# Optimization experiments

Hardware: AMD Instinct MI355X
Metric: run time of the kernel (lower is better)

Reference implementation:

```python
import jax, jax.numpy as jnp
import numpy as np

B, T, D, E = 2, 1653, 512, 8
D_E = D // E
BE = B * E


def setup_inputs() -> dict:
    key = jax.random.key(0)
    ks = jax.random.split(key, 11)
    s = 0.02  # keep linear-layer scale sane
    return {
        "input": jax.random.normal(ks[0], (B, T, D), jnp.float32),
        "Wq": jax.random.normal(ks[1], (D, D), jnp.float32) * s,
        "bq": jax.random.normal(ks[2], (D,), jnp.float32) * s,
        "Wk": jax.random.normal(ks[3], (D, D), jnp.float32) * s,
        "bk": jax.random.normal(ks[4], (D,), jnp.float32) * s,
        "Wv": jax.random.normal(ks[5], (D, D), jnp.float32) * s,
        "bv": jax.random.normal(ks[6], (D,), jnp.float32) * s,
        "Wo": jax.random.normal(ks[7], (D, D), jnp.float32) * s,
        "bo": jax.random.normal(ks[8], (D,), jnp.float32) * s,
        # random 'gaussian orthogonal punishment' matrix (diag(norms) @ blockwise-QR in torch; random here)
        "punish": jax.random.normal(ks[9], (T, T), jnp.float32) * (1.0 / np.sqrt(T)),
        # random tensor produced by torch.nn.init.orthogonal_(att_score) in the source
        "att_orth": jax.random.normal(ks[10], (BE, T, T), jnp.float32) * (1.0 / np.sqrt(T)),
    }


def _learnable_sigmoid(x):
    return 1.2 / (1.0 + jnp.exp(-1.6 * x))


def reference(input, Wq, bq, Wk, bk, Wv, bv, Wo, bo, punish, att_orth):
    # torch nn.Linear: y = x @ W^T + b
    def proj(W, b):
        # [B,T,D] -> permute(0,2,1) -> [B,D,T] -> reshape to [B*E, T, D_E]
        y = jnp.einsum('btd,ed->bte', input, W) + b
        return y.transpose(0, 2, 1).reshape(BE, T, D_E)

    Q = _learnable_sigmoid(proj(Wq, bq))            # [BE, T, D_E] (mask_q is all-ones => no-op)
    K = _learnable_sigmoid(proj(Wk, bk))            # [BE, T, D_E]
    V = proj(Wv, bv)                                # [BE, T, D_E]

    inv_sqrt_T = 1.0 / jnp.sqrt(jnp.float32(T))
    att = jnp.einsum('btd,bsd->bts', Q, K) * inv_sqrt_T  # [BE, T, T]

    # punishment: elementwise mul by broadcast punish matrix, then matmul with
    # the (transposed) random orthogonal tensor: att = (att * P) @ orth^T
    att = (att * punish[None, :, :]) @ att_orth.transpose(0, 2, 1)  # [BE, T, T]

    att = jnp.where(att == 0.0, jnp.float32(-2e20), att)  # masked_fill(att==0, -2e20)

    out = jnp.einsum('bts,bsd->btd', att, V)        # [BE, T, D_E]
    # permute(0,2,1) -> [BE, D_E, T] -> reshape [B, D, T] -> permute -> [B, T, D]
    out = out.transpose(0, 2, 1).reshape(B, D, T).transpose(0, 2, 1)
    return jnp.einsum('btd,ed->bte', out, Wo) + bo   # [B, T, D]
```

## Files before the change

kernel.cpp:

```cpp
#include <hip/hip_runtime.h>

#define TT 1653
#define DD 512
#define BB 2
#define DE 64
#define BEH 16
#define TTILES 26
#define TPAD 1664
#define SQN 26
#define NJC 4
#define MPSTRIDE TPAD

typedef __attribute__((ext_vector_type(8))) short bf16x8;
typedef __attribute__((ext_vector_type(4))) float f32x4;
typedef float f32x4u  __attribute__((ext_vector_type(4), aligned(4)));

__device__ __forceinline__ short f2bf(float f) {
    union { float f; unsigned u; } v; v.f = f;
    unsigned r = v.u + 0x7fffu + ((v.u >> 16) & 1u);
    return (short)(r >> 16);
}
__device__ __forceinline__ unsigned pack2(float a, float b) {
    return (unsigned)(unsigned short)f2bf(a) | ((unsigned)(unsigned short)f2bf(b) << 16);
}
__device__ __forceinline__ float bf2f(short s) {
    union { unsigned u; float f; } v; v.u = ((unsigned)(unsigned short)s) << 16;
    return v.f;
}

__global__ __launch_bounds__(256) void convp2_kernel(
    const float* __restrict__ P, short* __restrict__ Pbf)
{
    const int g = blockIdx.x * 256 + threadIdx.x;
    const int NG4 = TPAD / 4;
    if (g >= TT * NG4) return;
    const int r = g / NG4, c4 = (g - r * NG4) * 4;
    float p0 = 0.f, p1 = 0.f, p2 = 0.f, p3 = 0.f;
    const float* prow = P + (size_t)r * TT;
    if (c4 + 0 < TT) p0 = prow[c4 + 0];
    if (c4 + 1 < TT) p1 = prow[c4 + 1];
    if (c4 + 2 < TT) p2 = prow[c4 + 2];
    if (c4 + 3 < TT) p3 = prow[c4 + 3];
    uint2 o; o.x = pack2(p0, p1); o.y = pack2(p2, p3);
    *(uint2*)(Pbf + (size_t)r * TPAD + c4) = o;
}

__global__ __launch_bounds__(256) void proj3_kernel(
    const float* __restrict__ X,
    const float* __restrict__ W0, const float* __restrict__ b0,
    const float* __restrict__ W1, const float* __restrict__ b1,
    const float* __restrict__ W2, const float* __restrict__ b2,
    short* __restrict__ Y0, short* __restrict__ Y1, short* __restrict__ Y2)
{
    __shared__ __align__(16) short Wsh[64][72];
    __shared__ __align__(16) short Xs[64][72];

    const int tt = blockIdx.x, dt = blockIdx.y, z = blockIdx.z;
    const int b = z / 3, which = z % 3;
    const float* W    = (which == 0) ? W0 : (which == 1) ? W1 : W2;
    const float* bias = (which == 0) ? b0 : (which == 1) ? b1 : b2;
    short* Y          = (which == 0) ? Y0 : (which == 1) ? Y1 : Y2;

    const int t0 = tt * 64, d0 = dt * 64;
    const float* Xb = X + (size_t)b * TT * DD;

    const int tid  = threadIdx.x;
    const int wave = tid >> 6, lane = tid & 63;
    const int quad = lane >> 4, l16 = lane & 15;
    const int srow = tid >> 2, scg = (tid & 3) * 16;

    f32x4 acc[4];
    #pragma unroll
    for (int i = 0; i < 4; ++i) acc[i] = (f32x4){0.f, 0.f, 0.f, 0.f};

    float4 w0, w1, w2, w3, x0, x1, x2, x3;

    auto stage = [&](int k0) {
        const float* wrow = W + (size_t)(d0 + srow) * DD + k0 + scg;
        w0 = *(const float4*)(wrow);
        w1 = *(const float4*)(wrow + 4);
        w2 = *(const float4*)(wrow + 8);
        w3 = *(const float4*)(wrow + 12);
        const int t = t0 + srow;
        x0 = make_float4(0.f,0.f,0.f,0.f); x1 = x0; x2 = x0; x3 = x0;
        if (t < TT) {
            const float* xrow = Xb + (size_t)t * DD + k0 + scg;
            x0 = *(const float4*)(xrow);
            x1 = *(const float4*)(xrow + 4);
            x2 = *(const float4*)(xrow + 8);
            x3 = *(const float4*)(xrow + 12);
        }
    };
    auto lds_write = [&]() {
        uint4 pw0, pw1, px0, px1;
        pw0.x = pack2(w0.x, w0.y); pw0.y = pack2(w0.z, w0.w);
        pw0.z = pack2(w1.x, w1.y); pw0.w = pack2(w1.z, w1.w);
        pw1.x = pack2(w2.x, w2.y); pw1.y = pack2(w2.z, w2.w);
        pw1.z = pack2(w3.x, w3.y); pw1.w = pack2(w3.z, w3.w);
        px0.x = pack2(x0.x, x0.y); px0.y = pack2(x0.z, x0.w);
        px0.z = pack2(x1.x, x1.y); px0.w = pack2(x1.z, x1.w);
        px1.x = pack2(x2.x, x2.y); px1.y = pack2(x2.z, x2.w);
        px1.z = pack2(x3.x, x3.y); px1.w = pack2(x3.z, x3.w);
        *(uint4*)&Wsh[srow][scg]     = pw0;
        *(uint4*)&Wsh[srow][scg + 8] = pw1;
        *(uint4*)&Xs[srow][scg]      = px0;
        *(uint4*)&Xs[srow][scg + 8]  = px1;
    };

    stage(0);
    for (int k0 = 0; k0 < DD; k0 += 64) {
        if (k0) __syncthreads();
        lds_write();
        if (k0 + 64 < DD) stage(k0 + 64);
        __syncthreads();

        #pragma unroll
        for (int ks = 0; ks < 2; ++ks) {
            bf16x8 a = *(const bf16x8*)&Wsh[wave * 16 + l16][ks * 32 + quad * 8];
            #pragma unroll
            for (int nt = 0; nt < 4; ++nt) {
                bf16x8 bb = *(const bf16x8*)&Xs[nt * 16 + l16][ks * 32 + quad * 8];
                acc[nt] = __builtin_amdgcn_mfma_f32_16x16x32_bf16(a, bb, acc[nt], 0, 0, 0);
            }
        }
    }

    #pragma unroll
    for (int nt = 0; nt < 4; ++nt) {
        const int t = t0 + nt * 16 + l16;
        if (t < TT) {
            #pragma unroll
            for (int r = 0; r < 4; ++r) {
                const int d = d0 + wave * 16 + quad * 4 + r;
                float v = acc[nt][r] + bias[d];
                if (which < 2) v = 1.2f / (1.0f + __expf(-1.6f * v));
                Y[((size_t)b * DD + d) * TT + t] = f2bf(v);
            }
        }
    }
}

struct OVStage {
    f32x4u o0a, o0b, o1a, o1b;
    uint2  v0a, v0b, v1a, v1b;
};

__global__ __launch_bounds__(256, 4) void ovt5_kernel(
    const float* __restrict__ orth, const short* __restrict__ Vb,
    float* __restrict__ Mpart)
{
    __shared__ __align__(16) short Os[64][72];
    __shared__ __align__(16) short Vs[64][72];

    const int sq = blockIdx.x, be = blockIdx.y, jc = blockIdx.z;
    const int s0 = sq * 64;
    const int jt0 = (jc < 2) ? jc * 7 : 14 + (jc - 2) * 6;
    const int jtn = (jc < 2) ? 7 : 6;

    const float* O  = orth + (size_t)be * TT * TT;
    const short* Vh = Vb + (size_t)be * DE * TT;

    const int tid  = threadIdx.x;
    const int wave = tid >> 6, lane = tid & 63;
    const int quad = lane >> 4, l16 = lane & 15;

    const int p  = tid & 15;
    const int sc = tid >> 4;
    const int ca = s0 + 4 * sc;
    const bool fastS = (s0 + 64 <= TT);

    f32x4 acc[4];
    #pragma unroll
    for (int i = 0; i < 4; ++i) acc[i] = (f32x4){0.f, 0.f, 0.f, 0.f};

    auto stage_load = [&](OVStage& S, int j0) {
        const int jA = j0 + 2 * p;
        const int r0  = min(jA,      TT - 1);
        const int r0b = min(jA + 1,  TT - 1);
        const int r1  = min(jA + 32, TT - 1);
        const int r1b = min(jA + 33, TT - 1);
        if (fastS) {
            S.o0a = *(const f32x4u*)(O + (size_t)r0  * TT + ca);
            S.o0b = *(const f32x4u*)(O + (size_t)r0b * TT + ca);
            S.o1a = *(const f32x4u*)(O + (size_t)r1  * TT + ca);
            S.o1b = *(const f32x4u*)(O + (size_t)r1b * TT + ca);
        } else {
            #pragma unroll
            for (int i = 0; i < 4; ++i) {
                const int col = ca + i;
                const bool cv = (col < TT);
                S.o0a[i] = cv ? O[(size_t)r0  * TT + col] : 0.f;
                S.o0b[i] = cv ? O[(size_t)r0b * TT + col] : 0.f;
                S.o1a[i] = cv ? O[(size_t)r1  * TT + col] : 0.f;
                S.o1b[i] = cv ? O[(size_t)r1b * TT + col] : 0.f;
            }
        }
        const uint2 z = make_uint2(0u, 0u);
        S.v0a = (jA      < TT) ? *(const uint2*)(Vh + (size_t)jA       * DE + 4 * sc) : z;
        S.v0b = (jA + 1  < TT) ? *(const uint2*)(Vh + (size_t)(jA + 1) * DE + 4 * sc) : z;
        S.v1a = (jA + 32 < TT) ? *(const uint2*)(Vh + (size_t)(jA + 32)* DE + 4 * sc) : z;
        S.v1b = (jA + 33 < TT) ? *(const uint2*)(Vh + (size_t)(jA + 33)* DE + 4 * sc) : z;
    };

    auto lds_write = [&](const OVStage& S) {
        #pragma unroll
        for (int i = 0; i < 4; ++i) {
            *(unsigned*)&Os[4 * sc + i][2 * p]      = pack2(S.o0a[i], S.o0b[i]);
            *(unsigned*)&Os[4 * sc + i][2 * p + 32] = pack2(S.o1a[i], S.o1b[i]);
        }
        *(unsigned*)&Vs[4 * sc + 0][2 * p]      = (S.v0a.x & 0xffffu) | (S.v0b.x << 16);
        *(unsigned*)&Vs[4 * sc + 1][2 * p]      = (S.v0a.x >> 16)     | (S.v0b.x & 0xffff0000u);
        *(unsigned*)&Vs[4 * sc + 2][2 * p]      = (S.v0a.y & 0xffffu) | (S.v0b.y << 16);
        *(unsigned*)&Vs[4 * sc + 3][2 * p]      = (S.v0a.y >> 16)     | (S.v0b.y & 0xffff0000u);
        *(unsigned*)&Vs[4 * sc + 0][2 * p + 32] = (S.v1a.x & 0xffffu) | (S.v1b.x << 16);
        *(unsigned*)&Vs[4 * sc + 1][2 * p + 32] = (S.v1a.x >> 16)     | (S.v1b.x & 0xffff0000u);
        *(unsigned*)&Vs[4 * sc + 2][2 * p + 32] = (S.v1a.y & 0xffffu) | (S.v1b.y << 16);
        *(unsigned*)&Vs[4 * sc + 3][2 * p + 32] = (S.v1a.y >> 16)     | (S.v1b.y & 0xffff0000u);
    };

    auto mfma_tile = [&]() {
        #pragma unroll
        for (int ks = 0; ks < 2; ++ks) {
            bf16x8 bb = *(const bf16x8*)&Os[wave * 16 + l16][ks * 32 + quad * 8];
            #pragma unroll
            for (int i = 0; i < 4; ++i) {
                bf16x8 a = *(const bf16x8*)&Vs[i * 16 + l16][ks * 32 + quad * 8];
                acc[i] = __builtin_amdgcn_mfma_f32_16x16x32_bf16(a, bb, acc[i], 0, 0, 0);
            }
        }
    };

    OVStage sA, sB;
    stage_load(sA, (jt0 + 0) * 64);
    if (jtn > 1) stage_load(sB, (jt0 + 1) * 64);

    for (int t = 0; t < jtn; t += 2) {
        if (t) __syncthreads();
        lds_write(sA);
        if (t + 2 < jtn) stage_load(sA, (jt0 + t + 2) * 64);
        __syncthreads();
        mfma_tile();
        if (t + 1 < jtn) {
            __syncthreads();
            lds_write(sB);
            if (t + 3 < jtn) stage_load(sB, (jt0 + t + 3) * 64);
            __syncthreads();
            mfma_tile();
        }
    }

    float* Mp = Mpart + (size_t)(jc * BEH + be) * DE * MPSTRIDE;
    const int s = s0 + wave * 16 + l16;
    #pragma unroll
    for (int i = 0; i < 4; ++i) {
        #pragma unroll
        for (int r = 0; r < 4; ++r) {
            const int d = i * 16 + quad * 4 + r;
            Mp[(size_t)d * MPSTRIDE + s] = acc[i][r];
        }
    }
}

__global__ __launch_bounds__(256) void mreduce_kernel(
    const float* __restrict__ Mpart, short* __restrict__ Mt)
{
    const int g = blockIdx.x * 256 + threadIdx.x;
    const int NG = TPAD / 4;
    if (g >= BEH * DE * NG) return;
    const int bd = g / NG;
    const int s4 = (g - bd * NG) * 4;

    const size_t jstride = (size_t)BEH * DE * MPSTRIDE;
    const float* p = Mpart + (size_t)bd * MPSTRIDE + s4;
    float4 a0 = *(const float4*)(p);
    float4 a1 = *(const float4*)(p + jstride);
    float4 a2 = *(const float4*)(p + 2 * jstride);
    float4 a3 = *(const float4*)(p + 3 * jstride);
    float s0 = a0.x + a1.x + a2.x + a3.x;
    float s1 = a0.y + a1.y + a2.y + a3.y;
    float s2 = a0.z + a1.z + a2.z + a3.z;
    float s3 = a0.w + a1.w + a2.w + a3.w;

    uint2 o;
    o.x = pack2(s0, s1);
    o.y = pack2(s2, s3);
    *(uint2*)(Mt + (size_t)bd * TPAD + s4) = o;
}

struct AStage {
    uint4 k0, k1, m0, m1, p0, p1;
};

__global__ __launch_bounds__(256, 4) void attn3_kernel(
    const short* __restrict__ Qb, const short* __restrict__ Kb,
    const short* __restrict__ Mt, const short* __restrict__ Pbf,
    float* __restrict__ Hbuf)
{
    __shared__ __align__(16) short Qs[64][72];
    __shared__ __align__(16) short Ks[64][72];
    __shared__ __align__(16) short Ms[64][72];
    __shared__ __align__(16) short Ps[64][72];

    const int it = blockIdx.x, be = blockIdx.y;
    const int b = be >> 3, e = be & 7;
    const int i0 = it * 64;
    const short* Qh = Qb + (size_t)be * DE * TT;
    const short* Kh = Kb + (size_t)be * DE * TT;
    const short* Mh = Mt + (size_t)be * DE * TPAD;

    const int tid  = threadIdx.x;
    const int wave = tid >> 6, lane = tid & 63;
    const int quad = lane >> 4, l16 = lane & 15;

    const float invs = 0.024598297f;

    const int srow = tid >> 2, scg = (tid & 3) * 16;
    const int gi = i0 + srow;
    const bool giv = (gi < TT);

    {
        uint4 z = make_uint4(0u, 0u, 0u, 0u);
        uint4 v0 = z, v1 = z;
        if (giv) {
            v0 = *(const uint4*)(Qh + (size_t)gi * DE + scg);
            v1 = *(const uint4*)(Qh + (size_t)gi * DE + scg + 8);
        }
        *(uint4*)&Qs[srow][scg]     = v0;
        *(uint4*)&Qs[srow][scg + 8] = v1;
    }

    f32x4 out[4];
    #pragma unroll
    for (int i = 0; i < 4; ++i) out[i] = (f32x4){0.f, 0.f, 0.f, 0.f};

    auto stage_regs = [&](AStage& S, int s0) {
        const uint4 z = make_uint4(0u, 0u, 0u, 0u);
        const int gs = s0 + srow;
        S.k0 = z; S.k1 = z;
        if (gs < TT) {
            S.k0 = *(const uint4*)(Kh + (size_t)gs * DE + scg);
            S.k1 = *(const uint4*)(Kh + (size_t)gs * DE + scg + 8);
        }
        S.m0 = *(const uint4*)(Mh + (size_t)srow * TPAD + s0 + scg);
        S.m1 = *(const uint4*)(Mh + (size_t)srow * TPAD + s0 + scg + 8);
        S.p0 = z; S.p1 = z;
        if (giv) {
            S.p0 = *(const uint4*)(Pbf + (size_t)gi * TPAD + s0 + scg);
            S.p1 = *(const uint4*)(Pbf + (size_t)gi * TPAD + s0 + scg + 8);
        }
    };

    auto lds_write = [&](const AStage& S) {
        *(uint4*)&Ks[srow][scg]     = S.k0;
        *(uint4*)&Ks[srow][scg + 8] = S.k1;
        *(uint4*)&Ms[srow][scg]     = S.m0;
        *(uint4*)&Ms[srow][scg + 8] = S.m1;
        *(uint4*)&Ps[srow][scg]     = S.p0;
        *(uint4*)&Ps[srow][scg + 8] = S.p1;
    };

    auto compute = [&]() {
        f32x4 w[4];
        #pragma unroll
        for (int i = 0; i < 4; ++i) w[i] = (f32x4){0.f, 0.f, 0.f, 0.f};
        #pragma unroll
        for (int ks = 0; ks < 2; ++ks) {
            bf16x8 a = *(const bf16x8*)&Qs[wave * 16 + l16][ks * 32 + quad * 8];
            #pragma unroll
            for (int stile = 0; stile < 4; ++stile) {
                bf16x8 bb = *(const bf16x8*)&Ks[stile * 16 + l16][ks * 32 + quad * 8];
                w[stile] = __builtin_amdgcn_mfma_f32_16x16x32_bf16(a, bb, w[stile], 0, 0, 0);
            }
        }

        #pragma unroll
        for (int stile = 0; stile < 4; ++stile) {
            const int sl = stile * 16 + l16;
            #pragma unroll
            for (int r = 0; r < 4; ++r) {
                const int il = wave * 16 + quad * 4 + r;
                float v = w[stile][r] * invs * bf2f(Ps[il][sl]);
                Ps[il][sl] = f2bf(v);
            }
        }

        #pragma unroll
        for (int ks = 0; ks < 2; ++ks) {
            bf16x8 a = *(const bf16x8*)&Ps[wave * 16 + l16][ks * 32 + quad * 8];
            #pragma unroll
            for (int dt = 0; dt < 4; ++dt) {
                bf16x8 bb = *(const bf16x8*)&Ms[dt * 16 + l16][ks * 32 + quad * 8];
                out[dt] = __builtin_amdgcn_mfma_f32_16x16x32_bf16(a, bb, out[dt], 0, 0, 0);
            }
        }
    };

    AStage sA, sB;
    stage_regs(sA, 0);
    stage_regs(sB, 64);

    for (int tt = 0; tt < TTILES; tt += 2) {
        if (tt) __syncthreads();
        lds_write(sA);
        if (tt + 2 < TTILES) stage_regs(sA, (tt + 2) * 64);
        __syncthreads();
        compute();
        __syncthreads();
        lds_write(sB);
        if (tt + 3 < TTILES) stage_regs(sB, (tt + 3) * 64);
        __syncthreads();
        compute();
    }

    #pragma unroll
    for (int dt = 0; dt < 4; ++dt) {
        const int d = dt * 16 + l16;
        #pragma unroll
        for (int r = 0; r < 4; ++r) {
            const int go = i0 + wave * 16 + quad * 4 + r;
            if (go < TT)
                Hbuf[((size_t)b * TT + go) * DD + e * 64 + d] = out[dt][r];
        }
    }
}

__global__ __launch_bounds__(256) void oproj_kernel(
    const float* __restrict__ H, const float* __restrict__ Wo,
    const float* __restrict__ bo, float* __restrict__ out)
{
    __shared__ float Hs[16][68];
    __shared__ float Ns[16][68];

    const int tt = blockIdx.x, nt = blockIdx.y, b = blockIdx.z;
    const int t0 = tt * 64, n0 = nt * 64;
    const float* Hb = H + (size_t)b * TT * DD;

    const int tid = threadIdx.x;
    const int tx = tid & 15, ty = tid >> 4;
    const int lrow = tid >> 2, lq = tid & 3;
    const int trow = t0 + lrow;

    float acc[4][4] = {};

    for (int k0 = 0; k0 < DD; k0 += 16) {
        float4 hv = make_float4(0.f, 0.f, 0.f, 0.f);
        if (trow < TT)
            hv = *(const float4*)(Hb + (size_t)trow * DD + k0 + lq*4);
        float4 wv = *(const float4*)(Wo + (size_t)(n0 + lrow) * DD + k0 + lq*4);
        __syncthreads();
        Hs[lq*4+0][lrow] = hv.x; Hs[lq*4+1][lrow] = hv.y;
        Hs[lq*4+2][lrow] = hv.z; Hs[lq*4+3][lrow] = hv.w;
        Ns[lq*4+0][lrow] = wv.x; Ns[lq*4+1][lrow] = wv.y;
        Ns[lq*4+2][lrow] = wv.z; Ns[lq*4+3][lrow] = wv.w;
        __syncthreads();
        #pragma unroll
        for (int k = 0; k < 16; ++k) {
            float4 a4 = *(const float4*)(&Hs[k][ty*4]);
            float4 c4 = *(const float4*)(&Ns[k][tx*4]);
            float a[4] = {a4.x, a4.y, a4.z, a4.w};
            float c[4] = {c4.x, c4.y, c4.z, c4.w};
            #pragma unroll
            for (int i = 0; i < 4; ++i)
                #pragma unroll
                for (int j = 0; j < 4; ++j)
                    acc[i][j] = fmaf(a[i], c[j], acc[i][j]);
        }
        __syncthreads();
    }

    #pragma unroll
    for (int i = 0; i < 4; ++i) {
        const int t = t0 + ty*4 + i;
        if (t < TT) {
            float4 v;
            v.x = acc[i][0] + bo[n0 + tx*4 + 0];
            v.y = acc[i][1] + bo[n0 + tx*4 + 1];
            v.z = acc[i][2] + bo[n0 + tx*4 + 2];
            v.w = acc[i][3] + bo[n0 + tx*4 + 3];
            *(float4*)(out + ((size_t)b * TT + t) * DD + n0 + tx*4) = v;
        }
    }
}

extern "C" void kernel_launch(void* const* d_in, const int* in_sizes, int n_in,
                              void* d_out, int out_size, void* d_ws, size_t ws_size,
                              hipStream_t stream)
{
    (void)in_sizes; (void)n_in; (void)out_size; (void)ws_size;

    const float* X    = (const float*)d_in[0];
    const float* Wq   = (const float*)d_in[1];
    const float* bq   = (const float*)d_in[2];
    const float* Wk   = (const float*)d_in[3];
    const float* bk   = (const float*)d_in[4];
    const float* Wv   = (const float*)d_in[5];
    const float* bv   = (const float*)d_in[6];
    const float* Wo   = (const float*)d_in[7];
    const float* bo   = (const float*)d_in[8];
    const float* P    = (const float*)d_in[9];
    const float* orth = (const float*)d_in[10];
    float* out = (float*)d_out;

    char* ws = (char*)d_ws;
    const size_t SZH = (size_t)BB * DD * TT * sizeof(short);
    short* Qb  = (short*)(ws);
    short* Kb  = (short*)(ws + SZH);
    short* Vb  = (short*)(ws + 2 * SZH);
    short* Mtb = (short*)(ws + 3 * SZH);
    short* Pbf = (short*)(ws + 3 * SZH + (size_t)BEH * DE * TPAD * sizeof(short));
    char*  after_p = ws + 3 * SZH + (size_t)BEH * DE * TPAD * sizeof(short)
                        + (size_t)TT * TPAD * sizeof(short);
    float* Mpart = (float*)after_p;
    float* Hbuf  = (float*)after_p;

    dim3 blk(256);

    convp2_kernel<<<dim3((TT * (TPAD / 4) + 255) / 256), blk, 0, stream>>>(P, Pbf);

    dim3 g1(TTILES, DD / 64, BB * 3);
    proj3_kernel<<<g1, blk, 0, stream>>>(X, Wq, bq, Wk, bk, Wv, bv, Qb, Kb, Vb);

    dim3 g2(SQN, BEH, NJC);
    ovt5_kernel<<<g2, blk, 0, stream>>>(orth, Vb, Mpart);

    dim3 gr((BEH * DE * (TPAD / 4) + 255) / 256);
    mreduce_kernel<<<gr, blk, 0, stream>>>(Mpart, Mtb);

    dim3 g3(TTILES, BEH);
    attn3_kernel<<<g3, blk, 0, stream>>>(Qb, Kb, Mtb, Pbf, Hbuf);

    dim3 g4(TTILES, DD / 64, BB);
    oproj_kernel<<<g4, blk, 0, stream>>>(Hbuf, Wo, bo, out);
}
```

Baseline: 408.0 us.

## Use unconditional clamped loads and fenced raw barriers in GEMM pipelines

Result: no change. 406.5 us (-0.4%).

```diff
diff --git a/kernel.cpp b/kernel.cpp
--- a/kernel.cpp
+++ b/kernel.cpp
@@ -26,6 +26,18 @@
 __device__ __forceinline__ float bf2f(short s) {
     union { unsigned u; float f; } v; v.u = ((unsigned)(unsigned short)s) << 16;
     return v.f;
+}
+
+__device__ __forceinline__ void bar_fenced() {
+    __builtin_amdgcn_sched_barrier(0);
+    __builtin_amdgcn_s_barrier();
+    __builtin_amdgcn_sched_barrier(0);
+}
+__device__ __forceinline__ void lgkm0_bar() {
+    asm volatile("s_waitcnt lgkmcnt(0)" ::: "memory");
+    __builtin_amdgcn_sched_barrier(0);
+    __builtin_amdgcn_s_barrier();
+    __builtin_amdgcn_sched_barrier(0);
 }
 
 __global__ __launch_bounds__(256) void convp2_kernel(
@@ -45,7 +57,7 @@
     *(uint2*)(Pbf + (size_t)r * TPAD + c4) = o;
 }
 
-__global__ __launch_bounds__(256) void proj3_kernel(
+__global__ __launch_bounds__(256) void proj4_kernel(
     const float* __restrict__ X,
     const float* __restrict__ W0, const float* __restrict__ b0,
     const float* __restrict__ W1, const float* __restrict__ b1,
@@ -68,6 +80,8 @@
     const int wave = tid >> 6, lane = tid & 63;
     const int quad = lane >> 4, l16 = lane & 15;
     const int srow = tid >> 2, scg = (tid & 3) * 16;
+    const int trow = t0 + srow;
+    const int rx = min(trow, TT - 1);
 
     f32x4 acc[4];
     #pragma unroll
@@ -81,26 +95,26 @@
         w1 = *(const float4*)(wrow + 4);
         w2 = *(const float4*)(wrow + 8);
         w3 = *(const float4*)(wrow + 12);
-        const int t = t0 + srow;
-        x0 = make_float4(0.f,0.f,0.f,0.f); x1 = x0; x2 = x0; x3 = x0;
-        if (t < TT) {
-            const float* xrow = Xb + (size_t)t * DD + k0 + scg;
-            x0 = *(const float4*)(xrow);
-            x1 = *(const float4*)(xrow + 4);
-            x2 = *(const float4*)(xrow + 8);
-            x3 = *(const float4*)(xrow + 12);
-        }
+        const float* xrow = Xb + (size_t)rx * DD + k0 + scg;
+        x0 = *(const float4*)(xrow);
+        x1 = *(const float4*)(xrow + 4);
+        x2 = *(const float4*)(xrow + 8);
+        x3 = *(const float4*)(xrow + 12);
     };
     auto lds_write = [&]() {
+        const bool tv = (trow < TT);
+        float4 zz = make_float4(0.f, 0.f, 0.f, 0.f);
+        float4 y0 = tv ? x0 : zz, y1 = tv ? x1 : zz;
+        float4 y2 = tv ? x2 : zz, y3 = tv ? x3 : zz;
         uint4 pw0, pw1, px0, px1;
         pw0.x = pack2(w0.x, w0.y); pw0.y = pack2(w0.z, w0.w);
         pw0.z = pack2(w1.x, w1.y); pw0.w = pack2(w1.z, w1.w);
         pw1.x = pack2(w2.x, w2.y); pw1.y = pack2(w2.z, w2.w);
         pw1.z = pack2(w3.x, w3.y); pw1.w = pack2(w3.z, w3.w);
-        px0.x = pack2(x0.x, x0.y); px0.y = pack2(x0.z, x0.w);
-        px0.z = pack2(x1.x, x1.y); px0.w = pack2(x1.z, x1.w);
-        px1.x = pack2(x2.x, x2.y); px1.y = pack2(x2.z, x2.w);
-        px1.z = pack2(x3.x, x3.y); px1.w = pack2(x3.z, x3.w);
+        px0.x = pack2(y0.x, y0.y); px0.y = pack2(y0.z, y0.w);
+        px0.z = pack2(y1.x, y1.y); px0.w = pack2(y1.z, y1.w);
+        px1.x = pack2(y2.x, y2.y); px1.y = pack2(y2.z, y2.w);
+        px1.z = pack2(y3.x, y3.y); px1.w = pack2(y3.z, y3.w);
         *(uint4*)&Wsh[srow][scg]     = pw0;
         *(uint4*)&Wsh[srow][scg + 8] = pw1;
         *(uint4*)&Xs[srow][scg]      = px0;
@@ -109,10 +123,9 @@
 
     stage(0);
     for (int k0 = 0; k0 < DD; k0 += 64) {
-        if (k0) __syncthreads();
         lds_write();
         if (k0 + 64 < DD) stage(k0 + 64);
-        __syncthreads();
+        lgkm0_bar();
 
         #pragma unroll
         for (int ks = 0; ks < 2; ++ks) {
@@ -123,6 +136,7 @@
                 acc[nt] = __builtin_amdgcn_mfma_f32_16x16x32_bf16(a, bb, acc[nt], 0, 0, 0);
             }
         }
+        bar_fenced();
     }
 
     #pragma unroll
@@ -145,7 +159,7 @@
     uint2  v0a, v0b, v1a, v1b;
 };
 
-__global__ __launch_bounds__(256, 4) void ovt5_kernel(
+__global__ __launch_bounds__(256) void ovt6_kernel(
     const float* __restrict__ orth, const short* __restrict__ Vb,
     float* __restrict__ Mpart)
 {
@@ -195,27 +209,32 @@
                 S.o1b[i] = cv ? O[(size_t)r1b * TT + col] : 0.f;
             }
         }
-        const uint2 z = make_uint2(0u, 0u);
-        S.v0a = (jA      < TT) ? *(const uint2*)(Vh + (size_t)jA       * DE + 4 * sc) : z;
-        S.v0b = (jA + 1  < TT) ? *(const uint2*)(Vh + (size_t)(jA + 1) * DE + 4 * sc) : z;
-        S.v1a = (jA + 32 < TT) ? *(const uint2*)(Vh + (size_t)(jA + 32)* DE + 4 * sc) : z;
-        S.v1b = (jA + 33 < TT) ? *(const uint2*)(Vh + (size_t)(jA + 33)* DE + 4 * sc) : z;
-    };
-
-    auto lds_write = [&](const OVStage& S) {
+        S.v0a = *(const uint2*)(Vh + (size_t)r0  * DE + 4 * sc);
+        S.v0b = *(const uint2*)(Vh + (size_t)r0b * DE + 4 * sc);
+        S.v1a = *(const uint2*)(Vh + (size_t)r1  * DE + 4 * sc);
+        S.v1b = *(const uint2*)(Vh + (size_t)r1b * DE + 4 * sc);
+    };
+
+    auto lds_write = [&](const OVStage& S, int j0) {
+        const int jA = j0 + 2 * p;
         #pragma unroll
         for (int i = 0; i < 4; ++i) {
             *(unsigned*)&Os[4 * sc + i][2 * p]      = pack2(S.o0a[i], S.o0b[i]);
             *(unsigned*)&Os[4 * sc + i][2 * p + 32] = pack2(S.o1a[i], S.o1b[i]);
         }
-        *(unsigned*)&Vs[4 * sc + 0][2 * p]      = (S.v0a.x & 0xffffu) | (S.v0b.x << 16);
-        *(unsigned*)&Vs[4 * sc + 1][2 * p]      = (S.v0a.x >> 16)     | (S.v0b.x & 0xffff0000u);
-        *(unsigned*)&Vs[4 * sc + 2][2 * p]      = (S.v0a.y & 0xffffu) | (S.v0b.y << 16);
-        *(unsigned*)&Vs[4 * sc + 3][2 * p]      = (S.v0a.y >> 16)     | (S.v0b.y & 0xffff0000u);
-        *(unsigned*)&Vs[4 * sc + 0][2 * p + 32] = (S.v1a.x & 0xffffu) | (S.v1b.x << 16);
-        *(unsigned*)&Vs[4 * sc + 1][2 * p + 32] = (S.v1a.x >> 16)     | (S.v1b.x & 0xffff0000u);
-        *(unsigned*)&Vs[4 * sc + 2][2 * p + 32] = (S.v1a.y & 0xffffu) | (S.v1b.y << 16);
-        *(unsigned*)&Vs[4 * sc + 3][2 * p + 32] = (S.v1a.y >> 16)     | (S.v1b.y & 0xffff0000u);
+        const uint2 z = make_uint2(0u, 0u);
+        uint2 v0a = (jA      < TT) ? S.v0a : z;
+        uint2 v0b = (jA + 1  < TT) ? S.v0b : z;
+        uint2 v1a = (jA + 32 < TT) ? S.v1a : z;
+        uint2 v1b = (jA + 33 < TT) ? S.v1b : z;
+        *(unsigned*)&Vs[4 * sc + 0][2 * p]      = (v0a.x & 0xffffu) | (v0b.x << 16);
+        *(unsigned*)&Vs[4 * sc + 1][2 * p]      = (v0a.x >> 16)     | (v0b.x & 0xffff0000u);
+        *(unsigned*)&Vs[4 * sc + 2][2 * p]      = (v0a.y & 0xffffu) | (v0b.y << 16);
+        *(unsigned*)&Vs[4 * sc + 3][2 * p]      = (v0a.y >> 16)     | (v0b.y & 0xffff0000u);
+        *(unsigned*)&Vs[4 * sc + 0][2 * p + 32] = (v1a.x & 0xffffu) | (v1b.x << 16);
+        *(unsigned*)&Vs[4 * sc + 1][2 * p + 32] = (v1a.x >> 16)     | (v1b.x & 0xffff0000u);
+        *(unsigned*)&Vs[4 * sc + 2][2 * p + 32] = (v1a.y & 0xffffu) | (v1b.y << 16);
+        *(unsigned*)&Vs[4 * sc + 3][2 * p + 32] = (v1a.y >> 16)     | (v1b.y & 0xffff0000u);
     };
 
     auto mfma_tile = [&]() {
@@ -232,20 +251,20 @@
 
     OVStage sA, sB;
     stage_load(sA, (jt0 + 0) * 64);
-    if (jtn > 1) stage_load(sB, (jt0 + 1) * 64);
+    stage_load(sB, (jt0 + 1) * 64);
 
     for (int t = 0; t < jtn; t += 2) {
-        if (t) __syncthreads();
-        lds_write(sA);
+        lds_write(sA, (jt0 + t) * 64);
         if (t + 2 < jtn) stage_load(sA, (jt0 + t + 2) * 64);
-        __syncthreads();
+        lgkm0_bar();
         mfma_tile();
+        bar_fenced();
         if (t + 1 < jtn) {
-            __syncthreads();
-            lds_write(sB);
+            lds_write(sB, (jt0 + t + 1) * 64);
             if (t + 3 < jtn) stage_load(sB, (jt0 + t + 3) * 64);
-            __syncthreads();
+            lgkm0_bar();
             mfma_tile();
+            bar_fenced();
         }
     }
 
@@ -291,7 +310,7 @@
     uint4 k0, k1, m0, m1, p0, p1;
 };
 
-__global__ __launch_bounds__(256, 4) void attn3_kernel(
+__global__ __launch_bounds__(256) void attn4_kernel(
     const short* __restrict__ Qb, const short* __restrict__ Kb,
     const short* __restrict__ Mt, const short* __restrict__ Pbf,
     float* __restrict__ Hbuf)
@@ -317,14 +336,13 @@
     const int srow = tid >> 2, scg = (tid & 3) * 16;
     const int gi = i0 + srow;
     const bool giv = (gi < TT);
+    const int ri = min(gi, TT - 1);
 
     {
         uint4 z = make_uint4(0u, 0u, 0u, 0u);
-        uint4 v0 = z, v1 = z;
-        if (giv) {
-            v0 = *(const uint4*)(Qh + (size_t)gi * DE + scg);
-            v1 = *(const uint4*)(Qh + (size_t)gi * DE + scg + 8);
-        }
+        uint4 v0 = *(const uint4*)(Qh + (size_t)ri * DE + scg);
+        uint4 v1 = *(const uint4*)(Qh + (size_t)ri * DE + scg + 8);
+        if (!giv) { v0 = z; v1 = z; }
         *(uint4*)&Qs[srow][scg]     = v0;
         *(uint4*)&Qs[srow][scg + 8] = v1;
     }
@@ -334,29 +352,28 @@
     for (int i = 0; i < 4; ++i) out[i] = (f32x4){0.f, 0.f, 0.f, 0.f};
 
     auto stage_regs = [&](AStage& S, int s0) {
-        const uint4 z = make_uint4(0u, 0u, 0u, 0u);
         const int gs = s0 + srow;
-        S.k0 = z; S.k1 = z;
-        if (gs < TT) {
-            S.k0 = *(const uint4*)(Kh + (size_t)gs * DE + scg);
-            S.k1 = *(const uint4*)(Kh + (size_t)gs * DE + scg + 8);
-        }
+        const int rs = min(gs, TT - 1);
+        S.k0 = *(const uint4*)(Kh + (size_t)rs * DE + scg);
+        S.k1 = *(const uint4*)(Kh + (size_t)rs * DE + scg + 8);
         S.m0 = *(const uint4*)(Mh + (size_t)srow * TPAD + s0 + scg);
         S.m1 = *(const uint4*)(Mh + (size_t)srow * TPAD + s0 + scg + 8);
-        S.p0 = z; S.p1 = z;
-        if (giv) {
-            S.p0 = *(const uint4*)(Pbf + (size_t)gi * TPAD + s0 + scg);
-            S.p1 = *(const uint4*)(Pbf + (size_t)gi * TPAD + s0 + scg + 8);
-        }
-    };
-
-    auto lds_write = [&](const AStage& S) {
-        *(uint4*)&Ks[srow][scg]     = S.k0;
-        *(uint4*)&Ks[srow][scg + 8] = S.k1;
+        S.p0 = *(const uint4*)(Pbf + (size_t)ri * TPAD + s0 + scg);
+        S.p1 = *(const uint4*)(Pbf + (size_t)ri * TPAD + s0 + scg + 8);
+    };
+
+    auto lds_write = [&](const AStage& S, int s0) {
+        const int gs = s0 + srow;
+        const uint4 z = make_uint4(0u, 0u, 0u, 0u);
+        const bool kv = (gs < TT);
+        uint4 k0 = kv ? S.k0 : z, k1 = kv ? S.k1 : z;
+        uint4 p0 = giv ? S.p0 : z, p1 = giv ? S.p1 : z;
+        *(uint4*)&Ks[srow][scg]     = k0;
+        *(uint4*)&Ks[srow][scg + 8] = k1;
         *(uint4*)&Ms[srow][scg]     = S.m0;
         *(uint4*)&Ms[srow][scg + 8] = S.m1;
-        *(uint4*)&Ps[srow][scg]     = S.p0;
-        *(uint4*)&Ps[srow][scg + 8] = S.p1;
+        *(uint4*)&Ps[srow][scg]     = p0;
+        *(uint4*)&Ps[srow][scg + 8] = p1;
     };
 
     auto compute = [&]() {
@@ -398,18 +415,19 @@
     AStage sA, sB;
     stage_regs(sA, 0);
     stage_regs(sB, 64);
+    lgkm0_bar();
 
     for (int tt = 0; tt < TTILES; tt += 2) {
-        if (tt) __syncthreads();
-        lds_write(sA);
+        lds_write(sA, tt * 64);
         if (tt + 2 < TTILES) stage_regs(sA, (tt + 2) * 64);
-        __syncthreads();
+        lgkm0_bar();
         compute();
-        __syncthreads();
-        lds_write(sB);
+        bar_fenced();
+        lds_write(sB, (tt + 1) * 64);
         if (tt + 3 < TTILES) stage_regs(sB, (tt + 3) * 64);
-        __syncthreads();
+        lgkm0_bar();
         compute();
+        bar_fenced();
     }
 
     #pragma unroll
@@ -518,16 +536,16 @@
     convp2_kernel<<<dim3((TT * (TPAD / 4) + 255) / 256), blk, 0, stream>>>(P, Pbf);
 
     dim3 g1(TTILES, DD / 64, BB * 3);
-    proj3_kernel<<<g1, blk, 0, stream>>>(X, Wq, bq, Wk, bk, Wv, bv, Qb, Kb, Vb);
+    proj4_kernel<<<g1, blk, 0, stream>>>(X, Wq, bq, Wk, bk, Wv, bv, Qb, Kb, Vb);
 
     dim3 g2(SQN, BEH, NJC);
-    ovt5_kernel<<<g2, blk, 0, stream>>>(orth, Vb, Mpart);
+    ovt6_kernel<<<g2, blk, 0, stream>>>(orth, Vb, Mpart);
 
     dim3 gr((BEH * DE * (TPAD / 4) + 255) / 256);
     mreduce_kernel<<<gr, blk, 0, stream>>>(Mpart, Mtb);
 
     dim3 g3(TTILES, BEH);
-    attn3_kernel<<<g3, blk, 0, stream>>>(Qb, Kb, Mtb, Pbf, Hbuf);
+    attn4_kernel<<<g3, blk, 0, stream>>>(Qb, Kb, Mtb, Pbf, Hbuf);
 
     dim3 g4(TTILES, DD / 64, BB);
     oproj_kernel<<<g4, blk, 0, stream>>>(Hbuf, Wo, bo, out);
```
